# Kernel optimization log

Measured on AMD Instinct MI355X. Metric: run time of the kernel, lower is better.

Reference implementation:

```python
import jax, jax.numpy as jnp
import numpy as np

N = 100000   # nodes
E = 1600000  # edges (avg degree 16)
D = 128      # feature dim (layer_sizes = [128, 128, 128])


def setup_inputs() -> dict:
    key = jax.random.key(0)
    ks = jax.random.split(key, 8)
    s = 1.0 / np.sqrt(D)  # glorot-ish scale for linear weights
    return {
        "x": jax.random.normal(ks[0], (N, D), jnp.float32),
        "edge_index": jax.random.randint(ks[1], (2, E), 0, N, dtype=jnp.int32),
        "perturb_first": jax.random.normal(ks[2], (N, D), jnp.float32) * 0.01,
        "perturb_last": jax.random.normal(ks[3], (N, D), jnp.float32) * 0.01,
        "W1": jax.random.normal(ks[4], (D, D), jnp.float32) * s,
        "b1": jnp.zeros((D,), jnp.float32),
        "W2": jax.random.normal(ks[5], (D, D), jnp.float32) * s,
        "b2": jnp.zeros((D,), jnp.float32),
    }


def reference(x, edge_index, perturb_first, perturb_last, W1, b1, W2, b2):
    n = x.shape[0]
    # PyG GCNConv: add self-loops, symmetric deg^{-1/2} normalization.
    loop = jnp.arange(n, dtype=edge_index.dtype)
    src = jnp.concatenate([edge_index[0], loop])  # [E+N]
    dst = jnp.concatenate([edge_index[1], loop])  # [E+N]
    deg = jax.ops.segment_sum(jnp.ones(dst.shape[0], x.dtype), dst, num_segments=n)
    dinv = jnp.where(deg > 0, 1.0 / jnp.sqrt(deg), 0.0)
    norm = (dinv[src] * dinv[dst])[:, None]  # [E+N, 1]

    def gcn_conv(h, W, b):
        h = h @ W.T                                   # linear (bias-free), [N, D]
        msg = h[src] * norm                           # gather + scale, [E+N, D]
        out = jax.ops.segment_sum(msg, dst, num_segments=n)  # scatter-add
        return out + b

    # forward only runs model[0] and model[3] (the two GCNConv layers);
    # norms and PReLU are skipped by the original forward.
    h = gcn_conv(x, W1, b1) + perturb_first
    out = gcn_conv(h, W2, b2) + perturb_last
    return out
```

## Files before the change

kernel.cpp:

```cpp
#include <hip/hip_runtime.h>
#include <math.h>

#define D 128
#define WS_PAD 132

typedef short bf16x8 __attribute__((ext_vector_type(8)));
typedef float f32x4 __attribute__((ext_vector_type(4)));

__device__ __forceinline__ unsigned short f2bf(float f) {
  unsigned u = __float_as_uint(f);
  u += 0x7FFFu + ((u >> 16) & 1u);
  return (unsigned short)(u >> 16);
}

__device__ __forceinline__ float bf2f(unsigned short h) {
  return __uint_as_float(((unsigned)h) << 16);
}


__global__ __launch_bounds__(256) void count_deg_kernel(const int* __restrict__ dst, int E,
                                                        int* __restrict__ deg,
                                                        const float* __restrict__ W2,
                                                        unsigned short* __restrict__ W2bf,
                                                        const float* __restrict__ W1,
                                                        unsigned short* __restrict__ W1h,
                                                        unsigned short* __restrict__ W1l) {
  int nbe = (E + 255) >> 8;
  int b = blockIdx.x;
  if (b >= nbe) {
    if (W2bf == nullptr) return;
    int which = b - nbe;
    if (which < 8) {
      int t = which * 256 + threadIdx.x;
      #pragma unroll
      for (int q = 0; q < 2; ++q) {
        int idx = t + q * 2048;
        float4 w = ((const float4*)W2)[idx];
        ushort4 o;
        o.x = f2bf(w.x); o.y = f2bf(w.y); o.z = f2bf(w.z); o.w = f2bf(w.w);
        ((ushort4*)W2bf)[idx] = o;
      }
    } else {
      int t = (which - 8) * 256 + threadIdx.x;
      #pragma unroll
      for (int q = 0; q < 2; ++q) {
        int idx = t + q * 2048;
        float4 w = ((const float4*)W1)[idx];
        ushort4 hi, lo;
        hi.x = f2bf(w.x); lo.x = f2bf(w.x - bf2f(hi.x));
        hi.y = f2bf(w.y); lo.y = f2bf(w.y - bf2f(hi.y));
        hi.z = f2bf(w.z); lo.z = f2bf(w.z - bf2f(hi.z));
        hi.w = f2bf(w.w); lo.w = f2bf(w.w - bf2f(hi.w));
        ((ushort4*)W1h)[idx] = hi;
        ((ushort4*)W1l)[idx] = lo;
      }
    }
    return;
  }
  int e = b * 256 + threadIdx.x;
  if (e < E) atomicAdd(&deg[dst[e]], 1);
}


__global__ __launch_bounds__(256) void scan_blocksum_kernel(const int* __restrict__ deg, int n,
                                                            int* __restrict__ blockSums) {
  __shared__ int sm[256];
  int t = threadIdx.x;
  int i = blockIdx.x * 256 + t;
  sm[t] = (i < n) ? deg[i] : 0;
  __syncthreads();
  for (int off = 128; off > 0; off >>= 1) {
    if (t < off) sm[t] += sm[t + off];
    __syncthreads();
  }
  if (t == 0) blockSums[blockIdx.x] = sm[0];
}

__global__ __launch_bounds__(512) void scan_top_kernel(int* __restrict__ blockSums, int nb) {
  __shared__ int sm[512];
  int t = threadIdx.x;
  int v = (t < nb) ? blockSums[t] : 0;
  sm[t] = v;
  __syncthreads();
  for (int off = 1; off < 512; off <<= 1) {
    int x = (t >= off) ? sm[t - off] : 0;
    __syncthreads();
    sm[t] += x;
    __syncthreads();
  }
  if (t < nb) blockSums[t] = sm[t] - v;
}

__global__ __launch_bounds__(256) void scan_write_kernel(const int* __restrict__ deg, int n,
                                                         const int* __restrict__ blockSums,
                                                         int* __restrict__ ptr,
                                                         float* __restrict__ dinv) {
  __shared__ int sm[256];
  int t = threadIdx.x;
  int i = blockIdx.x * 256 + t;
  int v = (i < n) ? deg[i] : 0;
  sm[t] = v;
  __syncthreads();
  for (int off = 1; off < 256; off <<= 1) {
    int x = (t >= off) ? sm[t - off] : 0;
    __syncthreads();
    sm[t] += x;
    __syncthreads();
  }
  if (i < n) {
    ptr[i] = blockSums[blockIdx.x] + sm[t] - v;
    dinv[i] = 1.0f / sqrtf((float)(v + 1));
  }
}


__device__ __forceinline__ void gemm_body(const float* __restrict__ X,
                                          const float* __restrict__ W,
                                          const float* __restrict__ dinv,
                                          unsigned short* __restrict__ H, int n,
                                          int bid, int nblocks,
                                          float* __restrict__ Ws, float* __restrict__ Xs) {
  const int tid = threadIdx.x;
  const int tx = tid & 31;
  const int ty = tid >> 5;
  const int ntiles = (n + 31) >> 5;

  for (int tile = bid; tile < ntiles; tile += nblocks) {
    const int row0 = tile << 5;
    const int rows_here = min(32, n - row0);
    __syncthreads();
    {
      const float4* Xg = (const float4*)(X + (size_t)row0 * D);
      int tmax = rows_here * 32;
      for (int t = tid; t < tmax; t += 256) ((float4*)Xs)[t] = Xg[t];
    }
    float acc[4][4] = {{0.f}};
    #pragma unroll
    for (int kt = 0; kt < 128; kt += 64) {
      __syncthreads();
      for (int t = tid; t < 2048; t += 256) {
        int j  = t >> 4;
        int k4 = (t & 15) << 2;
        float4 w = ((const float4*)W)[j * 32 + (kt >> 2) + (t & 15)];
        Ws[(k4 + 0) * WS_PAD + j] = w.x;
        Ws[(k4 + 1) * WS_PAD + j] = w.y;
        Ws[(k4 + 2) * WS_PAD + j] = w.z;
        Ws[(k4 + 3) * WS_PAD + j] = w.w;
      }
      __syncthreads();
      #pragma unroll 4
      for (int k = 0; k < 64; ++k) {
        float4 w = *(const float4*)&Ws[k * WS_PAD + (tx << 2)];
        #pragma unroll
        for (int r = 0; r < 4; ++r) {
          float xv = Xs[(ty + 8 * r) * 128 + (kt + k)];
          acc[r][0] += xv * w.x;
          acc[r][1] += xv * w.y;
          acc[r][2] += xv * w.z;
          acc[r][3] += xv * w.w;
        }
      }
    }
    #pragma unroll
    for (int r = 0; r < 4; ++r) {
      int row = row0 + ty + 8 * r;
      if (row < n) {
        float s = dinv[row];
        unsigned h0 = f2bf(s * acc[r][0]);
        unsigned h1 = f2bf(s * acc[r][1]);
        unsigned h2 = f2bf(s * acc[r][2]);
        unsigned h3 = f2bf(s * acc[r][3]);
        ((uint2*)(H + (size_t)row * D))[tx] = make_uint2(h0 | (h1 << 16), h2 | (h3 << 16));
      }
    }
  }
}


__global__ __launch_bounds__(256) void fused_fill_gemm_kernel(
    const int* __restrict__ src, const int* __restrict__ dst,
    int* __restrict__ ptr, int* __restrict__ csr, int E,
    const float* __restrict__ X, const float* __restrict__ W,
    const float* __restrict__ dinv, unsigned short* __restrict__ H, int n) {
  __shared__ float Ws[64 * WS_PAD];
  __shared__ float Xs[32 * 128];
  int sub = blockIdx.x & 7;
  if (sub < 2) {
    int fb = (blockIdx.x >> 3) * 2 + sub;
    int stride = 512 * 256;
    for (int e = fb * 256 + threadIdx.x; e < E; e += stride) {
      int d = dst[e];
      int pos = atomicAdd(&ptr[d], 1);
      csr[pos] = src[e];
    }
  } else {
    int gb = (blockIdx.x >> 3) * 6 + (sub - 2);
    gemm_body(X, W, dinv, H, n, gb, 1536, Ws, Xs);
  }
}

__global__ __launch_bounds__(256) void gemm128_kernel(const float* __restrict__ X,
                                                      const float* __restrict__ W,
                                                      const float* __restrict__ dinv,
                                                      unsigned short* __restrict__ H, int n) {
  __shared__ float Ws[64 * WS_PAD];
  __shared__ float Xs[32 * 128];
  gemm_body(X, W, dinv, H, n, blockIdx.x, gridDim.x, Ws, Xs);
}


#define FUSED_GRID 2048
#define G1_PITCH 136

__global__ __launch_bounds__(256) void fused_fill_mfma_kernel(
    const int* __restrict__ src, const int* __restrict__ dst,
    int* __restrict__ ptr, int* __restrict__ csr, int E,
    const float* __restrict__ X,
    const unsigned short* __restrict__ W1h, const unsigned short* __restrict__ W1l,
    const float* __restrict__ dinv, unsigned short* __restrict__ H, int n) {
  __shared__ unsigned short Ths[32 * G1_PITCH];
  __shared__ unsigned short Tls[32 * G1_PITCH];
  int sub = blockIdx.x & 7;
  if (sub < 4) {
    int fb = (blockIdx.x >> 3) * 4 + sub;
    const long long T = 1024 * 256;
    long long t = fb * 256 + threadIdx.x;
    const bool al16 = ((E & 3) == 0);
    for (long long e0 = t * 8; e0 < E; e0 += T * 8) {
      if (e0 + 8 <= (long long)E && al16) {
        int4 d0 = ((const int4*)(dst + e0))[0];
        int4 d1 = ((const int4*)(dst + e0))[1];
        int4 s0 = ((const int4*)(src + e0))[0];
        int4 s1 = ((const int4*)(src + e0))[1];
        int p0 = atomicAdd(&ptr[d0.x], 1);
        int p1 = atomicAdd(&ptr[d0.y], 1);
        int p2 = atomicAdd(&ptr[d0.z], 1);
        int p3 = atomicAdd(&ptr[d0.w], 1);
        int p4 = atomicAdd(&ptr[d1.x], 1);
        int p5 = atomicAdd(&ptr[d1.y], 1);
        int p6 = atomicAdd(&ptr[d1.z], 1);
        int p7 = atomicAdd(&ptr[d1.w], 1);
        csr[p0] = s0.x; csr[p1] = s0.y; csr[p2] = s0.z; csr[p3] = s0.w;
        csr[p4] = s1.x; csr[p5] = s1.y; csr[p6] = s1.z; csr[p7] = s1.w;
      } else {
        for (long long e = e0; e < E && e < e0 + 8; ++e) {
          int d = dst[e];
          csr[atomicAdd(&ptr[d], 1)] = src[e];
        }
      }
    }
  } else {
    int gb = (blockIdx.x >> 3) * 4 + (sub - 4);
    const int tid = threadIdx.x;
    const int wv = tid >> 6;
    const int lane = tid & 63;
    const int m = lane & 15;
    const int quad = lane >> 4;
    const int mt = wv >> 1;
    const int ntb = (wv & 1) * 4;
    const int ntiles = (n + 31) >> 5;

    for (int tile = gb; tile < ntiles; tile += 1024) {
      const int row0 = tile << 5;
      const int rows_here = min(32, n - row0);
      __syncthreads();
      {
        const float4* Xg = (const float4*)(X + (size_t)row0 * D);
        int tmax = rows_here * 32;
        for (int t = tid; t < tmax; t += 256) {
          float4 xv = Xg[t];
          int r = t >> 5, c4 = (t & 31) << 2;
          ushort4 hi, lo;
          hi.x = f2bf(xv.x); lo.x = f2bf(xv.x - bf2f(hi.x));
          hi.y = f2bf(xv.y); lo.y = f2bf(xv.y - bf2f(hi.y));
          hi.z = f2bf(xv.z); lo.z = f2bf(xv.z - bf2f(hi.z));
          hi.w = f2bf(xv.w); lo.w = f2bf(xv.w - bf2f(hi.w));
          *(ushort4*)&Ths[r * G1_PITCH + c4] = hi;
          *(ushort4*)&Tls[r * G1_PITCH + c4] = lo;
        }
      }
      __syncthreads();

      f32x4 acc0 = {0.f, 0.f, 0.f, 0.f};
      f32x4 acc1 = {0.f, 0.f, 0.f, 0.f};
      f32x4 acc2 = {0.f, 0.f, 0.f, 0.f};
      f32x4 acc3 = {0.f, 0.f, 0.f, 0.f};
      #pragma unroll
      for (int s = 0; s < 4; ++s) {
        int k = (s << 5) + (quad << 3);
        bf16x8 ah = *(const bf16x8*)&Ths[(mt * 16 + m) * G1_PITCH + k];
        bf16x8 al = *(const bf16x8*)&Tls[(mt * 16 + m) * G1_PITCH + k];
        bf16x8 bh0 = *(const bf16x8*)&W1h[(size_t)((ntb + 0) * 16 + m) * 128 + k];
        bf16x8 bl0 = *(const bf16x8*)&W1l[(size_t)((ntb + 0) * 16 + m) * 128 + k];
        acc0 = __builtin_amdgcn_mfma_f32_16x16x32_bf16(ah, bh0, acc0, 0, 0, 0);
        acc0 = __builtin_amdgcn_mfma_f32_16x16x32_bf16(al, bh0, acc0, 0, 0, 0);
        acc0 = __builtin_amdgcn_mfma_f32_16x16x32_bf16(ah, bl0, acc0, 0, 0, 0);
        bf16x8 bh1 = *(const bf16x8*)&W1h[(size_t)((ntb + 1) * 16 + m) * 128 + k];
        bf16x8 bl1 = *(const bf16x8*)&W1l[(size_t)((ntb + 1) * 16 + m) * 128 + k];
        acc1 = __builtin_amdgcn_mfma_f32_16x16x32_bf16(ah, bh1, acc1, 0, 0, 0);
        acc1 = __builtin_amdgcn_mfma_f32_16x16x32_bf16(al, bh1, acc1, 0, 0, 0);
        acc1 = __builtin_amdgcn_mfma_f32_16x16x32_bf16(ah, bl1, acc1, 0, 0, 0);
        bf16x8 bh2 = *(const bf16x8*)&W1h[(size_t)((ntb + 2) * 16 + m) * 128 + k];
        bf16x8 bl2 = *(const bf16x8*)&W1l[(size_t)((ntb + 2) * 16 + m) * 128 + k];
        acc2 = __builtin_amdgcn_mfma_f32_16x16x32_bf16(ah, bh2, acc2, 0, 0, 0);
        acc2 = __builtin_amdgcn_mfma_f32_16x16x32_bf16(al, bh2, acc2, 0, 0, 0);
        acc2 = __builtin_amdgcn_mfma_f32_16x16x32_bf16(ah, bl2, acc2, 0, 0, 0);
        bf16x8 bh3 = *(const bf16x8*)&W1h[(size_t)((ntb + 3) * 16 + m) * 128 + k];
        bf16x8 bl3 = *(const bf16x8*)&W1l[(size_t)((ntb + 3) * 16 + m) * 128 + k];
        acc3 = __builtin_amdgcn_mfma_f32_16x16x32_bf16(ah, bh3, acc3, 0, 0, 0);
        acc3 = __builtin_amdgcn_mfma_f32_16x16x32_bf16(al, bh3, acc3, 0, 0, 0);
        acc3 = __builtin_amdgcn_mfma_f32_16x16x32_bf16(ah, bl3, acc3, 0, 0, 0);
      }
      #pragma unroll
      for (int r = 0; r < 4; ++r) {
        int row = mt * 16 + (quad << 2) + r;
        int g = row0 + row;
        if (g < n) {
          float sc = dinv[g];
          H[(size_t)g * D + (ntb + 0) * 16 + m] = f2bf(sc * acc0[r]);
          H[(size_t)g * D + (ntb + 1) * 16 + m] = f2bf(sc * acc1[r]);
          H[(size_t)g * D + (ntb + 2) * 16 + m] = f2bf(sc * acc2[r]);
          H[(size_t)g * D + (ntb + 3) * 16 + m] = f2bf(sc * acc3[r]);
        }
      }
    }
  }
}


__device__ __forceinline__ void gather_row(const int* __restrict__ csr,
                                           const int* __restrict__ rend,
                                           const unsigned* __restrict__ Hu,
                                           int i, int lane, float& ax, float& ay) {
  int start = (i == 0) ? 0 : rend[i - 1];
  int end = rend[i];
  unsigned v = Hu[(size_t)i * 64 + lane];
  ax = __uint_as_float(v << 16);
  ay = __uint_as_float(v & 0xFFFF0000u);
  int e = start;
  for (; e + 8 <= end; e += 8) {
    unsigned w0 = Hu[(size_t)csr[e + 0] * 64 + lane];
    unsigned w1 = Hu[(size_t)csr[e + 1] * 64 + lane];
    unsigned w2 = Hu[(size_t)csr[e + 2] * 64 + lane];
    unsigned w3 = Hu[(size_t)csr[e + 3] * 64 + lane];
    unsigned w4 = Hu[(size_t)csr[e + 4] * 64 + lane];
    unsigned w5 = Hu[(size_t)csr[e + 5] * 64 + lane];
    unsigned w6 = Hu[(size_t)csr[e + 6] * 64 + lane];
    unsigned w7 = Hu[(size_t)csr[e + 7] * 64 + lane];
    ax += __uint_as_float(w0 << 16) + __uint_as_float(w1 << 16) +
          __uint_as_float(w2 << 16) + __uint_as_float(w3 << 16) +
          __uint_as_float(w4 << 16) + __uint_as_float(w5 << 16) +
          __uint_as_float(w6 << 16) + __uint_as_float(w7 << 16);
    ay += __uint_as_float(w0 & 0xFFFF0000u) + __uint_as_float(w1 & 0xFFFF0000u) +
          __uint_as_float(w2 & 0xFFFF0000u) + __uint_as_float(w3 & 0xFFFF0000u) +
          __uint_as_float(w4 & 0xFFFF0000u) + __uint_as_float(w5 & 0xFFFF0000u) +
          __uint_as_float(w6 & 0xFFFF0000u) + __uint_as_float(w7 & 0xFFFF0000u);
  }
  for (; e < end; ++e) {
    unsigned w = Hu[(size_t)csr[e] * 64 + lane];
    ax += __uint_as_float(w << 16);
    ay += __uint_as_float(w & 0xFFFF0000u);
  }
}


__global__ __launch_bounds__(256, 8) void gather_kernel(const int* __restrict__ csr,
                                                        const int* __restrict__ rend,
                                                        const float* __restrict__ dinv,
                                                        const unsigned* __restrict__ Hu,
                                                        const float* __restrict__ bias,
                                                        const float* __restrict__ perturb,
                                                        float* __restrict__ out, int n) {
  int i = (blockIdx.x << 2) + (threadIdx.x >> 6);
  if (i >= n) return;
  int lane = threadIdx.x & 63;
  float ax, ay;
  gather_row(csr, rend, Hu, i, lane, ax, ay);
  float di = dinv[i];
  float2 p = ((const float2*)(perturb + (size_t)i * D))[lane];
  float2 o;
  o.x = bias[2 * lane + 0] + p.x + di * ax;
  o.y = bias[2 * lane + 1] + p.y + di * ay;
  ((float2*)(out + (size_t)i * D))[lane] = o;
}


#define GG_PITCH 136

__global__ __launch_bounds__(512, 8) void gather_gemm_kernel(
    const int* __restrict__ csr, const int* __restrict__ rend,
    const float* __restrict__ dinv, const unsigned* __restrict__ Hu,
    const float* __restrict__ bias, const float* __restrict__ perturb,
    const unsigned short* __restrict__ W2bf, unsigned short* __restrict__ H2, int n) {
  __shared__ unsigned short Ts[32 * GG_PITCH];
  const int tid = threadIdx.x;
  const int wv = tid >> 6;
  const int lane = tid & 63;
  const int base = blockIdx.x << 5;

  #pragma unroll
  for (int j = 0; j < 4; ++j) {
    int row = (wv << 2) + j;
    int i = base + row;
    if (i < n) {
      float ax, ay;
      gather_row(csr, rend, Hu, i, lane, ax, ay);
      float di = dinv[i];
      float2 p = ((const float2*)(perturb + (size_t)i * D))[lane];
      float ox = bias[2 * lane + 0] + p.x + di * ax;
      float oy = bias[2 * lane + 1] + p.y + di * ay;
      unsigned pack = (unsigned)f2bf(ox) | ((unsigned)f2bf(oy) << 16);
      *(unsigned*)&Ts[row * GG_PITCH + (lane << 1)] = pack;
    }
  }
  __syncthreads();

  const int mt = wv >> 2;
  const int nt0 = wv & 3;
  const int m = lane & 15;
  const int quad = lane >> 4;
  const unsigned short* Wrow0 = W2bf + (size_t)(nt0 * 16 + m) * 128;
  const unsigned short* Wrow1 = W2bf + (size_t)((nt0 + 4) * 16 + m) * 128;
  f32x4 acc0 = {0.f, 0.f, 0.f, 0.f};
  f32x4 acc1 = {0.f, 0.f, 0.f, 0.f};
  #pragma unroll
  for (int s = 0; s < 4; ++s) {
    int k = (s << 5) + (quad << 3);
    bf16x8 a  = *(const bf16x8*)&Ts[(mt * 16 + m) * GG_PITCH + k];
    bf16x8 b0 = *(const bf16x8*)&Wrow0[k];
    bf16x8 b1 = *(const bf16x8*)&Wrow1[k];
    acc0 = __builtin_amdgcn_mfma_f32_16x16x32_bf16(a, b0, acc0, 0, 0, 0);
    acc1 = __builtin_amdgcn_mfma_f32_16x16x32_bf16(a, b1, acc1, 0, 0, 0);
  }
  #pragma unroll
  for (int r = 0; r < 4; ++r) {
    int row = mt * 16 + (quad << 2) + r;
    int g = base + row;
    if (g < n) {
      float s = dinv[g];
      H2[(size_t)g * D + nt0 * 16 + m]       = f2bf(s * acc0[r]);
      H2[(size_t)g * D + (nt0 + 4) * 16 + m] = f2bf(s * acc1[r]);
    }
  }
}


extern "C" void kernel_launch(void* const* d_in, const int* in_sizes, int n_in,
                              void* d_out, int out_size, void* d_ws, size_t ws_size,
                              hipStream_t stream) {
  const float* x  = (const float*)d_in[0];
  const int*   ei = (const int*)d_in[1];
  const float* pf = (const float*)d_in[2];
  const float* pl = (const float*)d_in[3];
  const float* W1 = (const float*)d_in[4];
  const float* b1 = (const float*)d_in[5];
  const float* W2 = (const float*)d_in[6];
  const float* b2 = (const float*)d_in[7];
  float* out = (float*)d_out;

  const int n = in_sizes[0] / D;
  const int E = in_sizes[1] / 2;
  const int* src = ei;
  const int* dst = ei + E;

  int*   deg       = (int*)d_ws;
  float* dinv      = (float*)d_ws + n;
  int*   ptr       = (int*)d_ws + 2 * n;
  int*   blockSums = (int*)d_ws + 3 * n;
  int*   csr       = (int*)d_ws + 3 * n + 512;
  size_t a1_off = ((size_t)(3 * n + 512 + E) * 4 + 255) & ~(size_t)255;
  unsigned short* A1 = (unsigned short*)((char*)d_ws + a1_off);
  unsigned short* A2 = A1 + (size_t)n * D;
  unsigned short* W2bf = A2 + (size_t)n * D;
  unsigned short* W1h  = W2bf + 128 * 128;
  unsigned short* W1l  = W1h + 128 * 128;
  size_t needed = a1_off + (2 * (size_t)n * D + 3 * 128 * 128) * sizeof(unsigned short);
  const bool fused_l2 = (ws_size >= needed);

  const int nb_n = (n + 255) / 256;
  const int nb_e = (E + 255) / 256;
  const int nb_g = (n + 3) / 4;

  hipMemsetAsync(deg, 0, (size_t)n * sizeof(int), stream);
  count_deg_kernel<<<nb_e + 16, 256, 0, stream>>>(
      dst, E, deg, W2, fused_l2 ? W2bf : (unsigned short*)nullptr, W1, W1h, W1l);
  scan_blocksum_kernel<<<nb_n, 256, 0, stream>>>(deg, n, blockSums);
  scan_top_kernel<<<1, 512, 0, stream>>>(blockSums, nb_n);
  scan_write_kernel<<<nb_n, 256, 0, stream>>>(deg, n, blockSums, ptr, dinv);

  if (fused_l2) {
    fused_fill_mfma_kernel<<<FUSED_GRID, 256, 0, stream>>>(src, dst, ptr, csr, E, x, W1h, W1l,
                                                           dinv, A1, n);
    gather_gemm_kernel<<<(n + 31) / 32, 512, 0, stream>>>(csr, ptr, dinv, (const unsigned*)A1,
                                                          b1, pf, W2bf, A2, n);
    gather_kernel<<<nb_g, 256, 0, stream>>>(csr, ptr, dinv, (const unsigned*)A2, b2, pl, out, n);
  } else {
    fused_fill_gemm_kernel<<<FUSED_GRID, 256, 0, stream>>>(src, dst, ptr, csr, E, x, W1, dinv, A1, n);
    gather_kernel<<<nb_g, 256, 0, stream>>>(csr, ptr, dinv, (const unsigned*)A1, b1, pf, out, n);
    gemm128_kernel<<<1024, 256, 0, stream>>>(out, W2, dinv, A1, n);
    gather_kernel<<<nb_g, 256, 0, stream>>>(csr, ptr, dinv, (const unsigned*)A1, b2, pl, out, n);
  }
}
```

Baseline: 559.7 us.

## Record per-edge rank during degree count to make CSR fill atomic-free

The degree-count kernel now saves the atomicAdd return value as each edge's rank within its destination. The CSR fill then computes positions as ptr[dst]+rank with plain loads instead of a second round of atomics. The scan writes ptr[n] so the gather kernels read start/end from rptr[i], rptr[i+1]. The fill/GEMM block split also shifts from 4:4 to 2:6. This costs an extra E-int rank write and read, stored in the A2 buffer, and keeps an old gather kernel for the fallback path.

```diff
diff --git a/kernel.cpp b/kernel.cpp
--- a/kernel.cpp
+++ b/kernel.cpp
@@ -20,12 +20,13 @@
 
 __global__ __launch_bounds__(256) void count_deg_kernel(const int* __restrict__ dst, int E,
                                                         int* __restrict__ deg,
+                                                        int* __restrict__ rank,
                                                         const float* __restrict__ W2,
                                                         unsigned short* __restrict__ W2bf,
                                                         const float* __restrict__ W1,
                                                         unsigned short* __restrict__ W1h,
                                                         unsigned short* __restrict__ W1l) {
-  int nbe = (E + 255) >> 8;
+  int nbe = (E + 1023) >> 10;
   int b = blockIdx.x;
   if (b >= nbe) {
     if (W2bf == nullptr) return;
@@ -57,8 +58,21 @@
     }
     return;
   }
-  int e = b * 256 + threadIdx.x;
-  if (e < E) atomicAdd(&deg[dst[e]], 1);
+  int e0 = (b * 256 + threadIdx.x) * 4;
+  if (rank != nullptr) {
+    if (e0 + 4 <= E && ((E & 3) == 0)) {
+      int4 d = *(const int4*)(dst + e0);
+      int r0 = atomicAdd(&deg[d.x], 1);
+      int r1 = atomicAdd(&deg[d.y], 1);
+      int r2 = atomicAdd(&deg[d.z], 1);
+      int r3 = atomicAdd(&deg[d.w], 1);
+      *(int4*)(rank + e0) = make_int4(r0, r1, r2, r3);
+    } else {
+      for (int e = e0; e < E && e < e0 + 4; ++e) rank[e] = atomicAdd(&deg[dst[e]], 1);
+    }
+  } else {
+    for (int e = e0; e < E && e < e0 + 4; ++e) atomicAdd(&deg[dst[e]], 1);
+  }
 }
 
 
@@ -108,8 +122,10 @@
     __syncthreads();
   }
   if (i < n) {
-    ptr[i] = blockSums[blockIdx.x] + sm[t] - v;
+    int ex = blockSums[blockIdx.x] + sm[t] - v;
+    ptr[i] = ex;
     dinv[i] = 1.0f / sqrtf((float)(v + 1));
+    if (i == n - 1) ptr[n] = ex + v;
   }
 }
 
@@ -214,43 +230,44 @@
 
 __global__ __launch_bounds__(256) void fused_fill_mfma_kernel(
     const int* __restrict__ src, const int* __restrict__ dst,
-    int* __restrict__ ptr, int* __restrict__ csr, int E,
+    const int* __restrict__ ptr, const int* __restrict__ rank,
+    int* __restrict__ csr, int E,
     const float* __restrict__ X,
     const unsigned short* __restrict__ W1h, const unsigned short* __restrict__ W1l,
     const float* __restrict__ dinv, unsigned short* __restrict__ H, int n) {
   __shared__ unsigned short Ths[32 * G1_PITCH];
   __shared__ unsigned short Tls[32 * G1_PITCH];
   int sub = blockIdx.x & 7;
-  if (sub < 4) {
-    int fb = (blockIdx.x >> 3) * 4 + sub;
-    const long long T = 1024 * 256;
-    long long t = fb * 256 + threadIdx.x;
+  if (sub < 2) {
+    int fb = (blockIdx.x >> 3) * 2 + sub;
+    const int T8 = 512 * 256 * 8;
+    int t = fb * 256 + threadIdx.x;
     const bool al16 = ((E & 3) == 0);
-    for (long long e0 = t * 8; e0 < E; e0 += T * 8) {
-      if (e0 + 8 <= (long long)E && al16) {
+    for (int e0 = t * 8; e0 < E; e0 += T8) {
+      if (e0 + 8 <= E && al16) {
         int4 d0 = ((const int4*)(dst + e0))[0];
         int4 d1 = ((const int4*)(dst + e0))[1];
         int4 s0 = ((const int4*)(src + e0))[0];
         int4 s1 = ((const int4*)(src + e0))[1];
-        int p0 = atomicAdd(&ptr[d0.x], 1);
-        int p1 = atomicAdd(&ptr[d0.y], 1);
-        int p2 = atomicAdd(&ptr[d0.z], 1);
-        int p3 = atomicAdd(&ptr[d0.w], 1);
-        int p4 = atomicAdd(&ptr[d1.x], 1);
-        int p5 = atomicAdd(&ptr[d1.y], 1);
-        int p6 = atomicAdd(&ptr[d1.z], 1);
-        int p7 = atomicAdd(&ptr[d1.w], 1);
+        int4 r0 = ((const int4*)(rank + e0))[0];
+        int4 r1 = ((const int4*)(rank + e0))[1];
+        int p0 = ptr[d0.x] + r0.x;
+        int p1 = ptr[d0.y] + r0.y;
+        int p2 = ptr[d0.z] + r0.z;
+        int p3 = ptr[d0.w] + r0.w;
+        int p4 = ptr[d1.x] + r1.x;
+        int p5 = ptr[d1.y] + r1.y;
+        int p6 = ptr[d1.z] + r1.z;
+        int p7 = ptr[d1.w] + r1.w;
         csr[p0] = s0.x; csr[p1] = s0.y; csr[p2] = s0.z; csr[p3] = s0.w;
         csr[p4] = s1.x; csr[p5] = s1.y; csr[p6] = s1.z; csr[p7] = s1.w;
       } else {
-        for (long long e = e0; e < E && e < e0 + 8; ++e) {
-          int d = dst[e];
-          csr[atomicAdd(&ptr[d], 1)] = src[e];
-        }
+        for (int e = e0; e < E && e < e0 + 8; ++e)
+          csr[ptr[dst[e]] + rank[e]] = src[e];
       }
     }
   } else {
-    int gb = (blockIdx.x >> 3) * 4 + (sub - 4);
+    int gb = (blockIdx.x >> 3) * 6 + (sub - 2);
     const int tid = threadIdx.x;
     const int wv = tid >> 6;
     const int lane = tid & 63;
@@ -260,7 +277,7 @@
     const int ntb = (wv & 1) * 4;
     const int ntiles = (n + 31) >> 5;
 
-    for (int tile = gb; tile < ntiles; tile += 1024) {
+    for (int tile = gb; tile < ntiles; tile += 1536) {
       const int row0 = tile << 5;
       const int rows_here = min(32, n - row0);
       __syncthreads();
@@ -328,12 +345,9 @@
 }
 
 
-__device__ __forceinline__ void gather_row(const int* __restrict__ csr,
-                                           const int* __restrict__ rend,
+__device__ __forceinline__ void gather_row(const int* __restrict__ csr, int start, int end,
                                            const unsigned* __restrict__ Hu,
                                            int i, int lane, float& ax, float& ay) {
-  int start = (i == 0) ? 0 : rend[i - 1];
-  int end = rend[i];
   unsigned v = Hu[(size_t)i * 64 + lane];
   ax = __uint_as_float(v << 16);
   ay = __uint_as_float(v & 0xFFFF0000u);
@@ -365,7 +379,7 @@
 
 
 __global__ __launch_bounds__(256, 8) void gather_kernel(const int* __restrict__ csr,
-                                                        const int* __restrict__ rend,
+                                                        const int* __restrict__ rptr,
                                                         const float* __restrict__ dinv,
                                                         const unsigned* __restrict__ Hu,
                                                         const float* __restrict__ bias,
@@ -375,7 +389,7 @@
   if (i >= n) return;
   int lane = threadIdx.x & 63;
   float ax, ay;
-  gather_row(csr, rend, Hu, i, lane, ax, ay);
+  gather_row(csr, rptr[i], rptr[i + 1], Hu, i, lane, ax, ay);
   float di = dinv[i];
   float2 p = ((const float2*)(perturb + (size_t)i * D))[lane];
   float2 o;
@@ -384,11 +398,32 @@
   ((float2*)(out + (size_t)i * D))[lane] = o;
 }
 
+__global__ __launch_bounds__(256, 8) void gather_kernel_old(const int* __restrict__ csr,
+                                                            const int* __restrict__ rend,
+                                                            const float* __restrict__ dinv,
+                                                            const unsigned* __restrict__ Hu,
+                                                            const float* __restrict__ bias,
+                                                            const float* __restrict__ perturb,
+                                                            float* __restrict__ out, int n) {
+  int i = (blockIdx.x << 2) + (threadIdx.x >> 6);
+  if (i >= n) return;
+  int lane = threadIdx.x & 63;
+  int start = (i == 0) ? 0 : rend[i - 1];
+  float ax, ay;
+  gather_row(csr, start, rend[i], Hu, i, lane, ax, ay);
+  float di = dinv[i];
+  float2 p = ((const float2*)(perturb + (size_t)i * D))[lane];
+  float2 o;
+  o.x = bias[2 * lane + 0] + p.x + di * ax;
+  o.y = bias[2 * lane + 1] + p.y + di * ay;
+  ((float2*)(out + (size_t)i * D))[lane] = o;
+}
+
 
 #define GG_PITCH 136
 
 __global__ __launch_bounds__(512, 8) void gather_gemm_kernel(
-    const int* __restrict__ csr, const int* __restrict__ rend,
+    const int* __restrict__ csr, const int* __restrict__ rptr,
     const float* __restrict__ dinv, const unsigned* __restrict__ Hu,
     const float* __restrict__ bias, const float* __restrict__ perturb,
     const unsigned short* __restrict__ W2bf, unsigned short* __restrict__ H2, int n) {
@@ -404,7 +439,7 @@
     int i = base + row;
     if (i < n) {
       float ax, ay;
-      gather_row(csr, rend, Hu, i, lane, ax, ay);
+      gather_row(csr, rptr[i], rptr[i + 1], Hu, i, lane, ax, ay);
       float di = dinv[i];
       float2 p = ((const float2*)(perturb + (size_t)i * D))[lane];
       float ox = bias[2 * lane + 0] + p.x + di * ax;
@@ -466,38 +501,40 @@
   int*   deg       = (int*)d_ws;
   float* dinv      = (float*)d_ws + n;
   int*   ptr       = (int*)d_ws + 2 * n;
-  int*   blockSums = (int*)d_ws + 3 * n;
-  int*   csr       = (int*)d_ws + 3 * n + 512;
-  size_t a1_off = ((size_t)(3 * n + 512 + E) * 4 + 255) & ~(size_t)255;
+  int*   blockSums = (int*)d_ws + 3 * n + 1;
+  int*   csr       = (int*)d_ws + 3 * n + 1 + 512;
+  size_t a1_off = ((size_t)(3 * n + 1 + 512 + E) * 4 + 255) & ~(size_t)255;
   unsigned short* A1 = (unsigned short*)((char*)d_ws + a1_off);
   unsigned short* A2 = A1 + (size_t)n * D;
   unsigned short* W2bf = A2 + (size_t)n * D;
   unsigned short* W1h  = W2bf + 128 * 128;
   unsigned short* W1l  = W1h + 128 * 128;
+  int* rank = (int*)A2;
   size_t needed = a1_off + (2 * (size_t)n * D + 3 * 128 * 128) * sizeof(unsigned short);
   const bool fused_l2 = (ws_size >= needed);
 
   const int nb_n = (n + 255) / 256;
-  const int nb_e = (E + 255) / 256;
+  const int nb_e4 = (E + 1023) / 1024;
   const int nb_g = (n + 3) / 4;
 
   hipMemsetAsync(deg, 0, (size_t)n * sizeof(int), stream);
-  count_deg_kernel<<<nb_e + 16, 256, 0, stream>>>(
-      dst, E, deg, W2, fused_l2 ? W2bf : (unsigned short*)nullptr, W1, W1h, W1l);
+  count_deg_kernel<<<nb_e4 + 16, 256, 0, stream>>>(
+      dst, E, deg, fused_l2 ? rank : (int*)nullptr, W2,
+      fused_l2 ? W2bf : (unsigned short*)nullptr, W1, W1h, W1l);
   scan_blocksum_kernel<<<nb_n, 256, 0, stream>>>(deg, n, blockSums);
   scan_top_kernel<<<1, 512, 0, stream>>>(blockSums, nb_n);
   scan_write_kernel<<<nb_n, 256, 0, stream>>>(deg, n, blockSums, ptr, dinv);
 
   if (fused_l2) {
-    fused_fill_mfma_kernel<<<FUSED_GRID, 256, 0, stream>>>(src, dst, ptr, csr, E, x, W1h, W1l,
-                                                           dinv, A1, n);
+    fused_fill_mfma_kernel<<<FUSED_GRID, 256, 0, stream>>>(src, dst, ptr, rank, csr, E, x,
+                                                           W1h, W1l, dinv, A1, n);
     gather_gemm_kernel<<<(n + 31) / 32, 512, 0, stream>>>(csr, ptr, dinv, (const unsigned*)A1,
                                                           b1, pf, W2bf, A2, n);
     gather_kernel<<<nb_g, 256, 0, stream>>>(csr, ptr, dinv, (const unsigned*)A2, b2, pl, out, n);
   } else {
     fused_fill_gemm_kernel<<<FUSED_GRID, 256, 0, stream>>>(src, dst, ptr, csr, E, x, W1, dinv, A1, n);
-    gather_kernel<<<nb_g, 256, 0, stream>>>(csr, ptr, dinv, (const unsigned*)A1, b1, pf, out, n);
+    gather_kernel_old<<<nb_g, 256, 0, stream>>>(csr, ptr, dinv, (const unsigned*)A1, b1, pf, out, n);
     gemm128_kernel<<<1024, 256, 0, stream>>>(out, W2, dinv, A1, n);
-    gather_kernel<<<nb_g, 256, 0, stream>>>(csr, ptr, dinv, (const unsigned*)A1, b2, pl, out, n);
-  }
-}
+    gather_kernel_old<<<nb_g, 256, 0, stream>>>(csr, ptr, dinv, (const unsigned*)A1, b2, pl, out, n);
+  }
+}
```

Measured after the change: 525.7 us. 1.06x faster.
